# Kernel optimization log

Hardware: AMD Instinct MI355X
Metric: run time of the kernel (lower is better)

The kernel has to match this reference:

```python
import jax, jax.numpy as jnp
import numpy as np

VOCAB = 100000
EMBED = 64
SENT = 20
MEM = 50
BATCH = 32
HOPS = 3
PAD_ID = 0


def position_encoding(sentence_size, embedding_size):
    # Section 4.1 of MemN2N paper, vectorized. Returns [sentence_size, embedding_size].
    i = np.arange(1, embedding_size + 1, dtype=np.float32)[:, None]   # [E,1]
    j = np.arange(1, sentence_size + 1, dtype=np.float32)[None, :]    # [1,S]
    enc = (i - (embedding_size + 1) / 2.0) * (j - (sentence_size + 1) / 2.0)
    enc = 1.0 + 4.0 * enc / embedding_size / sentence_size
    enc[:, -1] = 1.0
    return jnp.asarray(enc.T, dtype=jnp.float32)  # [S,E]


def setup_inputs() -> dict:
    key = jax.random.key(0)
    k1, k2, k3, k4 = jax.random.split(key, 4)
    stories = jax.random.randint(k1, (BATCH, MEM, SENT), 0, VOCAB, dtype=jnp.int64 if jax.config.jax_enable_x64 else jnp.int32)
    queries = jax.random.randint(k2, (BATCH, SENT), 0, VOCAB, dtype=jnp.int64 if jax.config.jax_enable_x64 else jnp.int32)
    A = jax.random.normal(k3, (VOCAB, EMBED), dtype=jnp.float32) * 0.1
    C = jax.random.normal(k4, (HOPS, VOCAB, EMBED), dtype=jnp.float32) * 0.1
    # padding_idx=PAD_ID rows are zero, as in nn.Embedding(padding_idx=...)
    A = A.at[PAD_ID].set(0.0)
    C = C.at[:, PAD_ID].set(0.0)
    encoding = position_encoding(SENT, EMBED)
    return {"stories": stories, "queries": queries, "A": A, "C": C, "encoding": encoding}


def reference(stories, queries, A, C, encoding):
    # queries: [B,S], stories: [B,M,S], A: [V,E], C: [hops,V,E], encoding: [S,E]
    q_emb = A[queries]                                # [B,S,E]
    u = (q_emb * encoding).sum(axis=1)                # [B,E]
    for hop in range(HOPS):
        table_in = A if hop == 0 else C[hop - 1]
        emb_A = table_in[stories]                     # [B,M,S,E]
        m = (emb_A * encoding).sum(axis=2)            # [B,M,E]
        dotted = jnp.einsum('bme,be->bm', m, u)       # [B,M]
        probs = jax.nn.softmax(dotted, axis=-1)       # [B,M]
        emb_C = C[hop][stories]                       # [B,M,S,E]
        c = (emb_C * encoding).sum(axis=2)            # [B,M,E]
        o = jnp.einsum('bm,bme->be', probs, c)        # [B,E]
        u = u + o
    return u @ C[-1].T                                # [B,V]
```

## Files before the change

kernel.cpp:

```cpp
#include <hip/hip_runtime.h>
#include <hip/hip_bf16.h>

#define VOCAB 100000
#define EMBED 64
#define SENT  20
#define MEM   50
#define BATCH 32
#define HOPS  3

#define NSET  4
#define NSLOT (NSET * BATCH * MEM)

__device__ __forceinline__ float bfr(unsigned short x) {
    union { unsigned int u; float f; } cv;
    cv.u = ((unsigned int)x) << 16;
    return cv.f;
}

__device__ __forceinline__ bool is_bf16(const void* enc) {
    return ((const unsigned int*)enc)[639] == 0x3F803F80u;
}

template<bool BF>
__device__ __forceinline__ float ldT(const void* p, size_t idx) {
    if constexpr (BF) return bfr(((const unsigned short*)p)[idx]);
    else              return ((const float*)p)[idx];
}

__device__ __forceinline__ float wave_sum(float d) {
#pragma unroll
    for (int off = 32; off > 0; off >>= 1) d += __shfl_xor(d, off, 64);
    return d;
}

template<bool BF>
__device__ __forceinline__ void gather_body(const int* __restrict__ stories,
                                            const int* __restrict__ queries,
                                            const void* __restrict__ A,
                                            const void* __restrict__ C,
                                            const void* __restrict__ enc,
                                            float* __restrict__ mc_ws,
                                            float* __restrict__ u0g)
{
    const int tid = threadIdx.x;
    const int e   = tid & 63;
    const int gw  = blockIdx.x * 4 + (tid >> 6);
    const size_t VE = (size_t)VOCAB * EMBED;

    float encr[SENT];
#pragma unroll
    for (int s = 0; s < SENT; ++s) encr[s] = ldT<BF>(enc, s * EMBED + e);

    if (gw < NSLOT) {
        const int t  = gw / (BATCH * MEM);
        const int bm = gw % (BATCH * MEM);
        const void* T   = (t == 0) ? A : C;
        const size_t to = (t == 0) ? 0 : (size_t)(t - 1) * VE;

        int wst = (e < SENT) ? stories[bm * SENT + e] : 0;
        float acc = 0.f;
#pragma unroll
        for (int s = 0; s < SENT; ++s) {
            int w = __shfl(wst, s, 64);
            acc += ldT<BF>(T, to + (size_t)w * EMBED + e) * encr[s];
        }
        mc_ws[gw * EMBED + e] = acc;
    } else if (gw < NSLOT + BATCH) {
        const int b = gw - NSLOT;
        int wq = (e < SENT) ? queries[b * SENT + e] : 0;
        float u = 0.f;
#pragma unroll
        for (int s = 0; s < SENT; ++s) {
            int w = __shfl(wq, s, 64);
            u += ldT<BF>(A, (size_t)w * EMBED + e) * encr[s];
        }
        u0g[b * EMBED + e] = u;
    }
}

__global__ __launch_bounds__(256) void k_gather(
    const int* __restrict__ stories,
    const int* __restrict__ queries,
    const void* __restrict__ A,
    const void* __restrict__ C,
    const void* __restrict__ enc,
    float* __restrict__ mc_ws,
    float* __restrict__ u0g)
{
    if (is_bf16(enc)) gather_body<true >(stories, queries, A, C, enc, mc_ws, u0g);
    else              gather_body<false>(stories, queries, A, C, enc, mc_ws, u0g);
}

__global__ __launch_bounds__(256) void k_recur2(
    const float* __restrict__ mc_ws,
    const float* __restrict__ u0g,
    float* __restrict__ u3g)
{
    const int b    = blockIdx.x;
    const int tid  = threadIdx.x;
    const int lane = tid & 63;
    const int widx = tid >> 6;

    __shared__ float mc[NSET][MEM][65];
    __shared__ float uls[EMBED];
    __shared__ float ols[4][EMBED];

    for (int idx = tid; idx < NSET * MEM * 16; idx += 256) {
        int t  = idx / (MEM * 16);
        int r  = idx % (MEM * 16);
        int mm = r >> 4;
        int e4 = r & 15;
        const float4 v = *(const float4*)(mc_ws +
            (((size_t)t * BATCH * MEM) + (size_t)b * MEM + mm) * EMBED + e4 * 4);
        mc[t][mm][e4 * 4 + 0] = v.x;
        mc[t][mm][e4 * 4 + 1] = v.y;
        mc[t][mm][e4 * 4 + 2] = v.z;
        mc[t][mm][e4 * 4 + 3] = v.w;
    }
    if (tid < EMBED) uls[tid] = u0g[b * EMBED + tid];
    __syncthreads();

    for (int hop = 0; hop < HOPS; ++hop) {
        float d = 0.f;
        if (lane < MEM) {
#pragma unroll
            for (int e = 0; e < EMBED; ++e)
                d += mc[hop][lane][e] * uls[e];
        }
        float x = (lane < MEM) ? d : -3.4e38f;
        float mx = x;
#pragma unroll
        for (int off = 32; off > 0; off >>= 1) mx = fmaxf(mx, __shfl_xor(mx, off, 64));
        float ex = (lane < MEM) ? __expf(x - mx) : 0.f;
        float sm = wave_sum(ex);
        float p = ex / sm;

        float o = 0.f;
#pragma unroll
        for (int k = 0; k < 13; ++k) {
            int mm = widx * 13 + k;
            if (mm < MEM)
                o += __shfl(p, mm, 64) * mc[hop + 1][mm][lane];
        }
        ols[widx][lane] = o;
        __syncthreads();
        if (tid < EMBED)
            uls[tid] += ols[0][tid] + ols[1][tid] + ols[2][tid] + ols[3][tid];
        __syncthreads();
    }

    if (tid < EMBED) u3g[b * EMBED + tid] = uls[tid];
}

template<bool BF>
__device__ __forceinline__ void out_body(const float* __restrict__ u,
                                         const void* __restrict__ Cbase,
                                         void* __restrict__ out, int v)
{
    const size_t c2_off = (size_t)2 * VOCAB * EMBED;
    float row[EMBED];
    if constexpr (BF) {
        const uint4* rp = (const uint4*)((const unsigned short*)Cbase + c2_off + (size_t)v * EMBED);
#pragma unroll
        for (int i = 0; i < 8; ++i) {
            uint4 r = rp[i];
            row[i*8 + 0] = bfr((unsigned short)(r.x & 0xffff));
            row[i*8 + 1] = bfr((unsigned short)(r.x >> 16));
            row[i*8 + 2] = bfr((unsigned short)(r.y & 0xffff));
            row[i*8 + 3] = bfr((unsigned short)(r.y >> 16));
            row[i*8 + 4] = bfr((unsigned short)(r.z & 0xffff));
            row[i*8 + 5] = bfr((unsigned short)(r.z >> 16));
            row[i*8 + 6] = bfr((unsigned short)(r.w & 0xffff));
            row[i*8 + 7] = bfr((unsigned short)(r.w >> 16));
        }
    } else {
        const float4* rp = (const float4*)((const float*)Cbase + c2_off + (size_t)v * EMBED);
#pragma unroll
        for (int i = 0; i < 16; ++i) {
            float4 r = rp[i];
            row[i*4 + 0] = r.x; row[i*4 + 1] = r.y;
            row[i*4 + 2] = r.z; row[i*4 + 3] = r.w;
        }
    }

    float res[BATCH];
#pragma unroll
    for (int bb = 0; bb < BATCH; ++bb) {
        const float4* sp = (const float4*)(u + bb * EMBED);
        float acc = 0.f;
#pragma unroll
        for (int e4 = 0; e4 < 16; ++e4) {
            float4 us = sp[e4];
            acc += row[e4*4+0]*us.x + row[e4*4+1]*us.y
                 + row[e4*4+2]*us.z + row[e4*4+3]*us.w;
        }
        res[bb] = acc;
    }

    if constexpr (BF) {
        unsigned short* ob = (unsigned short*)out;
#pragma unroll
        for (int bb = 0; bb < BATCH; ++bb) {
            __hip_bfloat16 h = __float2bfloat16(res[bb]);
            ob[(size_t)bb * VOCAB + v] = *(unsigned short*)&h;
        }
    } else {
        float* of = (float*)out;
#pragma unroll
        for (int bb = 0; bb < BATCH; ++bb)
            of[(size_t)bb * VOCAB + v] = res[bb];
    }
}

__global__ __launch_bounds__(256) void k_out(const float* __restrict__ u,
                                             const void* __restrict__ Cbase,
                                             const void* __restrict__ enc,
                                             void* __restrict__ out)
{
    const int v = blockIdx.x * 256 + threadIdx.x;
    if (v >= VOCAB) return;
    if (is_bf16(enc)) out_body<true >(u, Cbase, out, v);
    else              out_body<false>(u, Cbase, out, v);
}

extern "C" void kernel_launch(void* const* d_in, const int* in_sizes, int n_in,
                              void* d_out, int out_size, void* d_ws, size_t ws_size,
                              hipStream_t stream)
{
    const int*  stories = (const int*)d_in[0];
    const int*  queries = (const int*)d_in[1];
    const void* A       = d_in[2];
    const void* C       = d_in[3];
    const void* enc     = d_in[4];

    float* mc_ws = (float*)d_ws;
    float* u0g   = mc_ws + NSLOT * EMBED;
    float* u3g   = u0g + BATCH * EMBED;

    const int nwaves  = NSLOT + BATCH;
    const int nblocks = (nwaves + 3) / 4;

    k_gather<<<nblocks, 256, 0, stream>>>(stories, queries, A, C, enc, mc_ws, u0g);
    k_recur2<<<BATCH, 256, 0, stream>>>(mc_ws, u0g, u3g);
    k_out<<<(VOCAB + 255) / 256, 256, 0, stream>>>(u3g, C, enc, d_out);
}
```

Before: 179.3 us.

## Compute output projection with bf16 MFMA tiles and stage u in LDS

Replaces the per-thread scalar dot products of the final u @ C[-1]^T with a wave-level MFMA 16x16x32 bf16 path: each wave handles 16 vocab rows against all 32 batch rows, reading C rows as packed bf16 vectors. The recurrence kernel now also writes a bf16 copy of u for use as the MFMA A operand. The fp32 fallback path stages u in shared memory instead of re-reading it from global memory. This removes the scalar FMA cost and register-heavy row unpacking, but rounds u to bf16 before the matmul and changes the store pattern to 16-element strided bf16 writes.

```diff
diff --git a/kernel.cpp b/kernel.cpp
--- a/kernel.cpp
+++ b/kernel.cpp
@@ -10,6 +10,10 @@
 
 #define NSET  4
 #define NSLOT (NSET * BATCH * MEM)
+#define NVT   (VOCAB / 16)
+
+typedef __attribute__((ext_vector_type(8))) short short8v;
+typedef __attribute__((ext_vector_type(4))) float f32x4;
 
 __device__ __forceinline__ float bfr(unsigned short x) {
     union { unsigned int u; float f; } cv;
@@ -94,7 +98,8 @@
 __global__ __launch_bounds__(256) void k_recur2(
     const float* __restrict__ mc_ws,
     const float* __restrict__ u0g,
-    float* __restrict__ u3g)
+    float* __restrict__ u3g,
+    unsigned short* __restrict__ u3bf)
 {
     const int b    = blockIdx.x;
     const int tid  = threadIdx.x;
@@ -149,44 +154,39 @@
         __syncthreads();
     }
 
-    if (tid < EMBED) u3g[b * EMBED + tid] = uls[tid];
-}
-
-template<bool BF>
-__device__ __forceinline__ void out_body(const float* __restrict__ u,
-                                         const void* __restrict__ Cbase,
-                                         void* __restrict__ out, int v)
-{
+    if (tid < EMBED) {
+        float uv = uls[tid];
+        u3g[b * EMBED + tid] = uv;
+        __hip_bfloat16 h = __float2bfloat16(uv);
+        u3bf[b * EMBED + tid] = *(unsigned short*)&h;
+    }
+}
+
+__device__ __forceinline__ void out_f32(const float* __restrict__ u,
+                                        const void* __restrict__ Cbase,
+                                        void* __restrict__ out)
+{
+    if (blockIdx.x * 256 >= VOCAB) return;
+    __shared__ __align__(16) float su[BATCH * EMBED];
+    for (int i = threadIdx.x; i < BATCH * EMBED; i += 256) su[i] = u[i];
+    __syncthreads();
+    const int v = blockIdx.x * 256 + threadIdx.x;
+    if (v >= VOCAB) return;
+
     const size_t c2_off = (size_t)2 * VOCAB * EMBED;
     float row[EMBED];
-    if constexpr (BF) {
-        const uint4* rp = (const uint4*)((const unsigned short*)Cbase + c2_off + (size_t)v * EMBED);
-#pragma unroll
-        for (int i = 0; i < 8; ++i) {
-            uint4 r = rp[i];
-            row[i*8 + 0] = bfr((unsigned short)(r.x & 0xffff));
-            row[i*8 + 1] = bfr((unsigned short)(r.x >> 16));
-            row[i*8 + 2] = bfr((unsigned short)(r.y & 0xffff));
-            row[i*8 + 3] = bfr((unsigned short)(r.y >> 16));
-            row[i*8 + 4] = bfr((unsigned short)(r.z & 0xffff));
-            row[i*8 + 5] = bfr((unsigned short)(r.z >> 16));
-            row[i*8 + 6] = bfr((unsigned short)(r.w & 0xffff));
-            row[i*8 + 7] = bfr((unsigned short)(r.w >> 16));
-        }
-    } else {
-        const float4* rp = (const float4*)((const float*)Cbase + c2_off + (size_t)v * EMBED);
-#pragma unroll
-        for (int i = 0; i < 16; ++i) {
-            float4 r = rp[i];
-            row[i*4 + 0] = r.x; row[i*4 + 1] = r.y;
-            row[i*4 + 2] = r.z; row[i*4 + 3] = r.w;
-        }
-    }
-
-    float res[BATCH];
+    const float4* rp = (const float4*)((const float*)Cbase + c2_off + (size_t)v * EMBED);
+#pragma unroll
+    for (int i = 0; i < 16; ++i) {
+        float4 r = rp[i];
+        row[i*4 + 0] = r.x; row[i*4 + 1] = r.y;
+        row[i*4 + 2] = r.z; row[i*4 + 3] = r.w;
+    }
+
+    float* of = (float*)out;
 #pragma unroll
     for (int bb = 0; bb < BATCH; ++bb) {
-        const float4* sp = (const float4*)(u + bb * EMBED);
+        const float4* sp = (const float4*)(su + bb * EMBED);
         float acc = 0.f;
 #pragma unroll
         for (int e4 = 0; e4 < 16; ++e4) {
@@ -194,33 +194,60 @@
             acc += row[e4*4+0]*us.x + row[e4*4+1]*us.y
                  + row[e4*4+2]*us.z + row[e4*4+3]*us.w;
         }
-        res[bb] = acc;
-    }
-
-    if constexpr (BF) {
-        unsigned short* ob = (unsigned short*)out;
-#pragma unroll
-        for (int bb = 0; bb < BATCH; ++bb) {
-            __hip_bfloat16 h = __float2bfloat16(res[bb]);
-            ob[(size_t)bb * VOCAB + v] = *(unsigned short*)&h;
-        }
-    } else {
-        float* of = (float*)out;
-#pragma unroll
-        for (int bb = 0; bb < BATCH; ++bb)
-            of[(size_t)bb * VOCAB + v] = res[bb];
+        of[(size_t)bb * VOCAB + v] = acc;
+    }
+}
+
+__device__ __forceinline__ void out_mfma(const unsigned short* __restrict__ ubf,
+                                         const void* __restrict__ Cbase,
+                                         void* __restrict__ out)
+{
+    const int tid  = threadIdx.x;
+    const int tv   = blockIdx.x * 4 + (tid >> 6);
+    if (tv >= NVT) return;
+    const int lane = tid & 63;
+    const int l15  = lane & 15;
+    const int lh   = lane >> 4;
+
+    const unsigned short* c2 =
+        (const unsigned short*)Cbase + (size_t)2 * VOCAB * EMBED;
+
+    const short8v a00 = *(const short8v*)(ubf + ( 0 + l15) * EMBED +  0 + lh * 8);
+    const short8v a01 = *(const short8v*)(ubf + ( 0 + l15) * EMBED + 32 + lh * 8);
+    const short8v a10 = *(const short8v*)(ubf + (16 + l15) * EMBED +  0 + lh * 8);
+    const short8v a11 = *(const short8v*)(ubf + (16 + l15) * EMBED + 32 + lh * 8);
+
+    const unsigned short* brow = c2 + ((size_t)tv * 16 + l15) * EMBED + lh * 8;
+    const short8v b0 = *(const short8v*)(brow);
+    const short8v b1 = *(const short8v*)(brow + 32);
+
+    f32x4 acc0 = {0.f, 0.f, 0.f, 0.f};
+    f32x4 acc1 = {0.f, 0.f, 0.f, 0.f};
+    acc0 = __builtin_amdgcn_mfma_f32_16x16x32_bf16(a00, b0, acc0, 0, 0, 0);
+    acc0 = __builtin_amdgcn_mfma_f32_16x16x32_bf16(a01, b1, acc0, 0, 0, 0);
+    acc1 = __builtin_amdgcn_mfma_f32_16x16x32_bf16(a10, b0, acc1, 0, 0, 0);
+    acc1 = __builtin_amdgcn_mfma_f32_16x16x32_bf16(a11, b1, acc1, 0, 0, 0);
+
+    unsigned short* ob = (unsigned short*)out;
+    const int v = tv * 16 + l15;
+#pragma unroll
+    for (int j = 0; j < 4; ++j) {
+        const int br = lh * 4 + j;
+        __hip_bfloat16 h0 = __float2bfloat16(acc0[j]);
+        ob[(size_t)br * VOCAB + v] = *(unsigned short*)&h0;
+        __hip_bfloat16 h1 = __float2bfloat16(acc1[j]);
+        ob[(size_t)(16 + br) * VOCAB + v] = *(unsigned short*)&h1;
     }
 }
 
 __global__ __launch_bounds__(256) void k_out(const float* __restrict__ u,
+                                             const unsigned short* __restrict__ ubf,
                                              const void* __restrict__ Cbase,
                                              const void* __restrict__ enc,
                                              void* __restrict__ out)
 {
-    const int v = blockIdx.x * 256 + threadIdx.x;
-    if (v >= VOCAB) return;
-    if (is_bf16(enc)) out_body<true >(u, Cbase, out, v);
-    else              out_body<false>(u, Cbase, out, v);
+    if (is_bf16(enc)) out_mfma(ubf, Cbase, out);
+    else              out_f32(u, Cbase, out);
 }
 
 extern "C" void kernel_launch(void* const* d_in, const int* in_sizes, int n_in,
@@ -236,11 +263,14 @@
     float* mc_ws = (float*)d_ws;
     float* u0g   = mc_ws + NSLOT * EMBED;
     float* u3g   = u0g + BATCH * EMBED;
+    unsigned short* u3bf = (unsigned short*)(u3g + BATCH * EMBED);
 
     const int nwaves  = NSLOT + BATCH;
     const int nblocks = (nwaves + 3) / 4;
 
+    const int noutblk = (NVT + 3) / 4;
+
     k_gather<<<nblocks, 256, 0, stream>>>(stories, queries, A, C, enc, mc_ws, u0g);
-    k_recur2<<<BATCH, 256, 0, stream>>>(mc_ws, u0g, u3g);
-    k_out<<<(VOCAB + 255) / 256, 256, 0, stream>>>(u3g, C, enc, d_out);
-}
+    k_recur2<<<BATCH, 256, 0, stream>>>(mc_ws, u0g, u3g, u3bf);
+    k_out<<<noutblk, 256, 0, stream>>>(u3g, u3bf, C, enc, d_out);
+}
```

Result: faster. 158.6 us (-11.6%).
